# Performance work log

Measured on AMD Instinct MI355X. Metric: run time of the kernel, lower is better.

## Reference

```python
import jax, jax.numpy as jnp
import numpy as np

B, S, D = 4, 2048, 512
H, HD = 8, 64  # head_num, head_dim


def setup_inputs() -> dict:
    key = jax.random.key(0)
    ks = jax.random.split(key, 5)
    scale = 1.0 / np.sqrt(D)  # roughly xavier-scale
    return {
        "x": jax.random.normal(ks[0], (B, S, D), dtype=jnp.float32),
        "Wq": jax.random.normal(ks[1], (D, D), dtype=jnp.float32) * scale,
        "bq": jnp.zeros((D,), dtype=jnp.float32),
        "Wk": jax.random.normal(ks[2], (D, D), dtype=jnp.float32) * scale,
        "bk": jnp.zeros((D,), dtype=jnp.float32),
        "Wv": jax.random.normal(ks[3], (D, D), dtype=jnp.float32) * scale,
        "bv": jnp.zeros((D,), dtype=jnp.float32),
        "Wo": jax.random.normal(ks[4], (D, D), dtype=jnp.float32) * scale,
        "bo": jnp.zeros((D,), dtype=jnp.float32),
    }


def reference(x, Wq, bq, Wk, bk, Wv, bv, Wo, bo):
    b, s, _ = x.shape
    # torch Linear: y = x @ W.T + b; reshape to (b, heads, s, head_dim)
    def proj(W, bias):
        return (x @ W.T + bias).reshape(b, s, H, HD).transpose(0, 2, 1, 3)
    Q, K, V = proj(Wq, bq), proj(Wk, bk), proj(Wv, bv)
    inv_sqrt_dk = 1.0 / jnp.sqrt(jnp.float32(HD))
    scores = jnp.einsum("bhqd,bhkd->bhqk", Q, K) * inv_sqrt_dk
    attn = jax.nn.softmax(scores, axis=-1)  # F.softmax default -> last dim
    ctx = jnp.einsum("bhqk,bhkd->bhqd", attn, V)
    ctx = ctx.transpose(0, 2, 1, 3).reshape(b, s, D)
    return ctx @ Wo.T + bo
```

## Files before the change

### kernel.cpp

```cpp
#include <hip/hip_runtime.h>
#include <hip/hip_bf16.h>
#include <cstdint>
#include <cstddef>

#define S_LEN 2048
#define D_DIM 512
#define NHEAD 8
#define HDIM  64

typedef __attribute__((ext_vector_type(8)))  __bf16 b8;
typedef __attribute__((ext_vector_type(4)))  __bf16 b4;
typedef __attribute__((ext_vector_type(4)))  float  f4;
typedef __attribute__((ext_vector_type(16))) float  f16v;
typedef __attribute__((ext_vector_type(4)))  unsigned int u32x4;

#define AS_GLOBAL __attribute__((address_space(1)))
#define AS_LDS    __attribute__((address_space(3)))

__device__ __forceinline__ void load_lds16(const void* g, void* l) {
  __builtin_amdgcn_global_load_lds((const AS_GLOBAL void*)g, (AS_LDS void*)l, 16, 0, 0);
}

__device__ __forceinline__ f4 mfma16(b8 a, b8 b, f4 c) {
  return __builtin_amdgcn_mfma_f32_16x16x32_bf16(a, b, c, 0, 0, 0);
}
__device__ __forceinline__ f16v mfma32(b8 a, b8 b, f16v c) {
  return __builtin_amdgcn_mfma_f32_32x32x16_bf16(a, b, c, 0, 0, 0);
}

__device__ __forceinline__ float exp2v(float x) {
#if __has_builtin(__builtin_amdgcn_exp2f)
  return __builtin_amdgcn_exp2f(x);
#else
  float r; asm("v_exp_f32 %0, %1" : "=v"(r) : "v"(x)); return r;
#endif
}

__device__ __forceinline__ unsigned int pkbf(float lo, float hi_) {
  unsigned int r;
  asm("v_cvt_pk_bf16_f32 %0, %1, %2" : "=v"(r) : "v"(lo), "v"(hi_));
  return r;
}

__device__ __forceinline__ float xhalf_max(float v) {
  return fmaxf(v, __shfl_xor(v, 32));
}
__device__ __forceinline__ float xhalf_add(float v) {
  return v + __shfl_xor(v, 32);
}

__device__ __forceinline__ b8 lds_frag(const __bf16* base, int row, int bc) {
  return *reinterpret_cast<const b8*>((const char*)base + row * 128 + (bc ^ ((row & 7) << 4)));
}

__global__ __launch_bounds__(256) void cvt_kernel(const float* __restrict__ in,
                                                  __bf16* __restrict__ out) {
  int i = (blockIdx.x * 256 + threadIdx.x) * 4;
  float4 v = *reinterpret_cast<const float4*>(in + i);
  b4 o;
  o.x = (__bf16)v.x; o.y = (__bf16)v.y; o.z = (__bf16)v.z; o.w = (__bf16)v.w;
  *reinterpret_cast<b4*>(out + i) = o;
}

__global__ __launch_bounds__(256) void cvt_w_kernel(const float* __restrict__ w0, const float* __restrict__ w1,
                                                    const float* __restrict__ w2, const float* __restrict__ w3,
                                                    __bf16* o0, __bf16* o1, __bf16* o2, __bf16* o3) {
  const float* in = blockIdx.y == 0 ? w0 : blockIdx.y == 1 ? w1 : blockIdx.y == 2 ? w2 : w3;
  __bf16* out     = blockIdx.y == 0 ? o0 : blockIdx.y == 1 ? o1 : blockIdx.y == 2 ? o2 : o3;
  int i = (blockIdx.x * 256 + threadIdx.x) * 4;
  float4 v = *reinterpret_cast<const float4*>(in + i);
  b4 o;
  o.x = (__bf16)v.x; o.y = (__bf16)v.y; o.z = (__bf16)v.z; o.w = (__bf16)v.w;
  *reinterpret_cast<b4*>(out + i) = o;
}

__device__ __forceinline__ void gemm_core(const __bf16* __restrict__ A, const __bf16* __restrict__ W,
                                          int m0, int n0, __bf16* As, __bf16* Bs, f4 acc[4][4]) {
  const int t = threadIdx.x;
  const int lane = t & 63;
  const int w = t >> 6, wr = w >> 1, wc = w & 1;
  const f4 zero = {0.f, 0.f, 0.f, 0.f};
  #pragma unroll
  for (int mi = 0; mi < 4; ++mi)
    #pragma unroll
    for (int ni = 0; ni < 4; ++ni) acc[mi][ni] = zero;

  const char* Ab = (const char*)A;
  const char* Wb = (const char*)W;
  for (int kt = 0; kt < 512; kt += 64) {
    __syncthreads();
    #pragma unroll
    for (int i = 0; i < 4; ++i) {
      int o = i * 4096 + t * 16;
      int row = o >> 7, cb = o & 127;
      int scb = cb ^ ((row & 7) << 4);
      load_lds16(Ab + ((size_t)(m0 + row) * 512 + kt) * 2 + scb, (char*)As + o);
      load_lds16(Wb + ((size_t)(n0 + row) * 512 + kt) * 2 + scb, (char*)Bs + o);
    }
    __syncthreads();
    #pragma unroll
    for (int kk = 0; kk < 2; ++kk) {
      b8 af[4], bf[4];
      #pragma unroll
      for (int mi = 0; mi < 4; ++mi)
        af[mi] = lds_frag(As, wr * 64 + mi * 16 + (lane & 15), kk * 64 + ((lane >> 4) << 4));
      #pragma unroll
      for (int ni = 0; ni < 4; ++ni)
        bf[ni] = lds_frag(Bs, wc * 64 + ni * 16 + (lane & 15), kk * 64 + ((lane >> 4) << 4));
      #pragma unroll
      for (int mi = 0; mi < 4; ++mi)
        #pragma unroll
        for (int ni = 0; ni < 4; ++ni)
          acc[mi][ni] = mfma16(af[mi], bf[ni], acc[mi][ni]);
    }
  }
}

__global__ __launch_bounds__(256) void gemm_qkv_kernel(
    const __bf16* __restrict__ xb,
    const __bf16* __restrict__ wq, const __bf16* __restrict__ wk, const __bf16* __restrict__ wv,
    const float* __restrict__ bq, const float* __restrict__ bk, const float* __restrict__ bv,
    __bf16* Qo, __bf16* Ko, __bf16* Vo) {
  __shared__ __bf16 As[128 * 64];
  __shared__ __bf16 Bs[128 * 64];
  int z = blockIdx.z;
  const __bf16* W = z == 0 ? wq : (z == 1 ? wk : wv);
  const float* bias = z == 0 ? bq : (z == 1 ? bk : bv);
  __bf16* out = z == 0 ? Qo : (z == 1 ? Ko : Vo);
  const float sc = (z == 0) ? 0.18033688011112042f : 1.0f;
  int m0 = blockIdx.x * 128, n0 = blockIdx.y * 128;
  f4 acc[4][4];
  gemm_core(xb, W, m0, n0, As, Bs, acc);
  int t = threadIdx.x, lane = t & 63, w = t >> 6, wr = w >> 1, wc = w & 1;
  #pragma unroll
  for (int mi = 0; mi < 4; ++mi)
    #pragma unroll
    for (int ni = 0; ni < 4; ++ni)
      #pragma unroll
      for (int r = 0; r < 4; ++r) {
        int m = m0 + wr * 64 + mi * 16 + ((lane >> 4) << 2) + r;
        int n = n0 + wc * 64 + ni * 16 + (lane & 15);
        float v = (acc[mi][ni][r] + bias[n]) * sc;
        int b = m >> 11, s = m & 2047, h = n >> 6, hd = n & 63;
        out[(((size_t)(b * NHEAD + h)) * S_LEN + s) * HDIM + hd] = (__bf16)v;
      }
}

__global__ __launch_bounds__(256) void gemm_o_kernel(const __bf16* __restrict__ ctx,
                                                     const __bf16* __restrict__ wo,
                                                     const float* __restrict__ bo,
                                                     float* __restrict__ out) {
  __shared__ __bf16 As[128 * 64];
  __shared__ __bf16 Bs[128 * 64];
  int m0 = blockIdx.x * 128, n0 = blockIdx.y * 128;
  f4 acc[4][4];
  gemm_core(ctx, wo, m0, n0, As, Bs, acc);
  int t = threadIdx.x, lane = t & 63, w = t >> 6, wr = w >> 1, wc = w & 1;
  #pragma unroll
  for (int mi = 0; mi < 4; ++mi)
    #pragma unroll
    for (int ni = 0; ni < 4; ++ni)
      #pragma unroll
      for (int r = 0; r < 4; ++r) {
        int m = m0 + wr * 64 + mi * 16 + ((lane >> 4) << 2) + r;
        int n = n0 + wc * 64 + ni * 16 + (lane & 15);
        out[(size_t)m * D_DIM + n] = acc[mi][ni][r] + bo[n];
      }
}

__global__ __launch_bounds__(256) void transpose_v_kernel(const __bf16* __restrict__ V,
                                                          __bf16* __restrict__ Vt) {
  __shared__ __bf16 tile[64][72];
  int bh = blockIdx.y, s0 = blockIdx.x * 64;
  const __bf16* Vp = V + (size_t)bh * S_LEN * HDIM;
  __bf16* Vtp = Vt + (size_t)bh * HDIM * S_LEN;
  int t = threadIdx.x;
  #pragma unroll
  for (int i = 0; i < 4; ++i) {
    int q = t + i * 256;
    int row = q >> 4, c4 = (q & 15) * 4;
    b4 v = *reinterpret_cast<const b4*>(&Vp[(size_t)(s0 + row) * HDIM + c4]);
    *reinterpret_cast<b4*>(&tile[row][c4]) = v;
  }
  __syncthreads();
  #pragma unroll
  for (int i = 0; i < 4; ++i) {
    int q = t + i * 256;
    int d = q >> 4, s4 = (q & 15) * 4;
    b4 v;
    v.x = tile[s4 + 0][d]; v.y = tile[s4 + 1][d];
    v.z = tile[s4 + 2][d]; v.w = tile[s4 + 3][d];
    *reinterpret_cast<b4*>(&Vtp[(size_t)d * S_LEN + s0 + s4]) = v;
  }
}

#define NTG 16

#define MKFRAG(dst, st, base) do {                                   \
    unsigned int A0_ = pkbf((st)[(base)+0], (st)[(base)+1]);         \
    unsigned int A1_ = pkbf((st)[(base)+2], (st)[(base)+3]);         \
    unsigned int B0_ = pkbf((st)[(base)+4], (st)[(base)+5]);         \
    unsigned int B1_ = pkbf((st)[(base)+6], (st)[(base)+7]);         \
    asm("v_permlane32_swap_b32 %0, %1" : "+v"(A0_), "+v"(B0_));      \
    asm("v_permlane32_swap_b32 %0, %1" : "+v"(A1_), "+v"(B1_));      \
    u32x4 wv_; wv_.x = A0_; wv_.y = A1_; wv_.z = B0_; wv_.w = B1_;   \
    dst = __builtin_bit_cast(b8, wv_);                               \
  } while (0)

#define TILE(KO, VO) do {                                                     \
    f16v t0 = Z16, t1 = Z16;                                                  \
    __builtin_amdgcn_s_setprio(1);                                            \
    _Pragma("unroll")                                                         \
    for (int ks = 0; ks < 4; ++ks) {                                          \
      b8 kf0 = *reinterpret_cast<const AS_LDS b8*>(sb + koff[ks] + (KO));     \
      b8 kf1 = *reinterpret_cast<const AS_LDS b8*>(sb + koff[ks] + (KO) + 4096); \
      t0 = mfma32(kf0, qf[ks], t0);                                           \
      t1 = mfma32(kf1, qf[ks], t1);                                           \
    }                                                                         \
    __builtin_amdgcn_s_setprio(0);                                            \
    float a0 = fmaxf(fmaxf(t0[0], t0[8]),  fmaxf(t1[0], t1[8]));              \
    float a1 = fmaxf(fmaxf(t0[1], t0[9]),  fmaxf(t1[1], t1[9]));              \
    float a2 = fmaxf(fmaxf(t0[2], t0[10]), fmaxf(t1[2], t1[10]));             \
    float a3 = fmaxf(fmaxf(t0[3], t0[11]), fmaxf(t1[3], t1[11]));             \
    float a4 = fmaxf(fmaxf(t0[4], t0[12]), fmaxf(t1[4], t1[12]));             \
    float a5 = fmaxf(fmaxf(t0[5], t0[13]), fmaxf(t1[5], t1[13]));             \
    float a6 = fmaxf(fmaxf(t0[6], t0[14]), fmaxf(t1[6], t1[14]));             \
    float a7 = fmaxf(fmaxf(t0[7], t0[15]), fmaxf(t1[7], t1[15]));             \
    float mx = fmaxf(fmaxf(fmaxf(a0, a1), fmaxf(a2, a3)),                     \
                     fmaxf(fmaxf(a4, a5), fmaxf(a6, a7)));                    \
    mx = xhalf_max(mx);                                                       \
    if (!__all(mx - mr <= 11.5f)) {                                           \
      float mn = fmaxf(mr, mx);                                               \
      float al = exp2v(mr - mn);                                              \
      mr = mn; lsum *= al; o0 *= al; o1 *= al;                                \
    }                                                                         \
    _Pragma("unroll")                                                         \
    for (int r = 0; r < 16; ++r) t0[r] = exp2v(t0[r] - mr);                   \
    _Pragma("unroll")                                                         \
    for (int r = 0; r < 16; ++r) t1[r] = exp2v(t1[r] - mr);                   \
    {                                                                         \
      float p0 = (t0[0] + t1[0]) + (t0[8]  + t1[8]);                          \
      float p1 = (t0[1] + t1[1]) + (t0[9]  + t1[9]);                          \
      float p2 = (t0[2] + t1[2]) + (t0[10] + t1[10]);                         \
      float p3 = (t0[3] + t1[3]) + (t0[11] + t1[11]);                         \
      float p4 = (t0[4] + t1[4]) + (t0[12] + t1[12]);                         \
      float p5 = (t0[5] + t1[5]) + (t0[13] + t1[13]);                         \
      float p6 = (t0[6] + t1[6]) + (t0[14] + t1[14]);                         \
      float p7 = (t0[7] + t1[7]) + (t0[15] + t1[15]);                         \
      lsum += ((p0 + p1) + (p2 + p3)) + ((p4 + p5) + (p6 + p7));              \
    }                                                                         \
    __builtin_amdgcn_s_setprio(1);                                            \
    _Pragma("unroll")                                                         \
    for (int ks = 0; ks < 4; ++ks) {                                          \
      b8 pa;                                                                  \
      if (ks == 0)      MKFRAG(pa, t0, 0);                                    \
      else if (ks == 1) MKFRAG(pa, t0, 8);                                    \
      else if (ks == 2) MKFRAG(pa, t1, 0);                                    \
      else              MKFRAG(pa, t1, 8);                                    \
      b8 vf0 = *reinterpret_cast<const AS_LDS b8*>(sb + koff[ks] + (VO));     \
      b8 vf1 = *reinterpret_cast<const AS_LDS b8*>(sb + koff[ks] + (VO) + 4096); \
      o0 = mfma32(vf0, pa, o0);                                               \
      o1 = mfma32(vf1, pa, o1);                                               \
    }                                                                         \
    __builtin_amdgcn_s_setprio(0);                                            \
  } while (0)

__global__ __launch_bounds__(512, 4) void attn_kernel(const __bf16* __restrict__ Q,
                                                      const __bf16* __restrict__ K,
                                                      const __bf16* __restrict__ Vt,
                                                      __bf16* __restrict__ ctx) {
  __shared__ char smem_[65536];
  int t = threadIdx.x, lane = t & 63, w = t >> 6;
  int lane31 = lane & 31, hi = lane >> 5;
  int grp = w >> 2, qs = w & 3, t256 = t & 255;

  int bid = blockIdx.x;
  int nid = (bid & 7) * 64 + (bid >> 3);
  int bh = nid >> 4, qtile = nid & 15;
  int b = bh >> 3, h = bh & 7;
  int q = qtile * 128 + qs * 32 + lane31;
  const __bf16* Qp = Q + (size_t)bh * S_LEN * HDIM;
  const __bf16* Kp = K + (size_t)bh * S_LEN * HDIM;
  const __bf16* Vp = Vt + (size_t)bh * HDIM * S_LEN;
  const int kv0 = grp * (S_LEN / 2);

  b8 qf[4];
  #pragma unroll
  for (int ks = 0; ks < 4; ++ks)
    qf[ks] = *reinterpret_cast<const b8*>(&Qp[(size_t)q * HDIM + ks * 16 + hi * 8]);

  const AS_LDS char* sb = (const AS_LDS char*)smem_;
  unsigned koff[4];
  #pragma unroll
  for (int ks = 0; ks < 4; ++ks) {
    int bc = hi * 16 + ks * 32;
    koff[ks] = grp * 16384 + lane31 * 128 + (bc ^ ((lane31 & 7) << 4));
  }

  int oA = t256 * 16, oB = 4096 + t256 * 16;
  int rA = oA >> 7, rB = oB >> 7;
  int sA = (oA & 127) ^ ((rA & 7) << 4), sB = (oB & 127) ^ ((rB & 7) << 4);
  const char* KgA = (const char*)Kp + (size_t)(kv0 + rA) * 128 + sA;
  const char* KgB = (const char*)Kp + (size_t)(kv0 + rB) * 128 + sB;
  const char* VgA = (const char*)Vp + (size_t)rA * (S_LEN * 2) + (size_t)kv0 * 2 + sA;
  const char* VgB = (const char*)Vp + (size_t)rB * (S_LEN * 2) + (size_t)kv0 * 2 + sB;

  const f16v Z16 = {0,0,0,0,0,0,0,0,0,0,0,0,0,0,0,0};
  f16v o0 = Z16, o1 = Z16;
  float mr = -1e30f, lsum = 0.f;

  auto stage = [&](int buf) {
    char* ldsK = smem_ + grp * 16384 + buf * 8192;
    load_lds16(KgA, ldsK + oA);
    load_lds16(KgB, ldsK + oB);
    load_lds16(VgA, ldsK + 32768 + oA);
    load_lds16(VgB, ldsK + 32768 + oB);
    KgA += 8192; KgB += 8192; VgA += 128; VgB += 128;
  };

  stage(0);
  __syncthreads();

  #pragma unroll 1
  for (int it2 = 0; it2 < NTG / 2; ++it2) {
    stage(1);
    TILE(0, 32768);
    __syncthreads();
    if (it2 < NTG / 2 - 1) stage(0);
    TILE(8192, 40960);
    __syncthreads();
  }

  float l_own = xhalf_add(lsum);
  float* OL = (float*)smem_;
  float* ML = OL + 8192;
  if (grp == 1) {
    #pragma unroll
    for (int g = 0; g < 4; ++g)
      #pragma unroll
      for (int j = 0; j < 4; ++j) {
        int d = 8 * g + 4 * hi + j;
        OL[(qs * 64 + d) * 32 + lane31]      = o0[4 * g + j];
        OL[(qs * 64 + 32 + d) * 32 + lane31] = o1[4 * g + j];
      }
    if (hi == 0) { ML[qs * 32 + lane31] = mr; ML[128 + qs * 32 + lane31] = l_own; }
  }
  __syncthreads();
  if (grp == 0) {
    float m1 = ML[qs * 32 + lane31], l1 = ML[128 + qs * 32 + lane31];
    float mm = fmaxf(mr, m1);
    float s0 = exp2v(mr - mm), s1 = exp2v(m1 - mm);
    float inv = 1.0f / (l_own * s0 + l1 * s1);
    __bf16* cp = ctx + (size_t)b * S_LEN * D_DIM + (size_t)q * D_DIM + (size_t)h * HDIM;
    #pragma unroll
    for (int g = 0; g < 4; ++g) {
      b4 v0, v1;
      #pragma unroll
      for (int j = 0; j < 4; ++j) {
        int d = 8 * g + 4 * hi + j;
        v0[j] = (__bf16)((o0[4 * g + j] * s0 + OL[(qs * 64 + d) * 32 + lane31] * s1) * inv);
        v1[j] = (__bf16)((o1[4 * g + j] * s0 + OL[(qs * 64 + 32 + d) * 32 + lane31] * s1) * inv);
      }
      int d0 = 8 * g + 4 * hi;
      *reinterpret_cast<b4*>(cp + d0)      = v0;
      *reinterpret_cast<b4*>(cp + 32 + d0) = v1;
    }
  }
}

extern "C" void kernel_launch(void* const* d_in, const int* in_sizes, int n_in,
                              void* d_out, int out_size, void* d_ws, size_t ws_size,
                              hipStream_t stream) {
  const float* x  = (const float*)d_in[0];
  const float* Wq = (const float*)d_in[1];
  const float* bq = (const float*)d_in[2];
  const float* Wk = (const float*)d_in[3];
  const float* bk = (const float*)d_in[4];
  const float* Wv = (const float*)d_in[5];
  const float* bv = (const float*)d_in[6];
  const float* Wo = (const float*)d_in[7];
  const float* bo = (const float*)d_in[8];
  float* out = (float*)d_out;

  char* ws = (char*)d_ws;
  __bf16* xb   = (__bf16*)(ws);
  __bf16* wqb  = xb  + 4194304;
  __bf16* wkb  = wqb + 262144;
  __bf16* wvb  = wkb + 262144;
  __bf16* wob  = wvb + 262144;
  __bf16* Qb   = wob + 262144;
  __bf16* Kb   = Qb  + 4194304;
  __bf16* Vb   = Kb  + 4194304;
  __bf16* Vtb  = Vb  + 4194304;
  __bf16* ctxb = xb;

  cvt_kernel<<<dim3(4096), dim3(256), 0, stream>>>(x, xb);
  cvt_w_kernel<<<dim3(256, 4), dim3(256), 0, stream>>>(Wq, Wk, Wv, Wo, wqb, wkb, wvb, wob);
  gemm_qkv_kernel<<<dim3(64, 4, 3), dim3(256), 0, stream>>>(xb, wqb, wkb, wvb, bq, bk, bv, Qb, Kb, Vb);
  transpose_v_kernel<<<dim3(32, 32), dim3(256), 0, stream>>>(Vb, Vtb);
  attn_kernel<<<dim3(512), dim3(512), 0, stream>>>(Qb, Kb, Vtb, ctxb);
  gemm_o_kernel<<<dim3(64, 4), dim3(256), 0, stream>>>(ctxb, wob, bo, out);
}
```

Before: 102.0 us.

## Software-pipeline QK^T of next tile with softmax and PV of current tile

Splits the attention tile into a QK^T stage and a softmax+PV stage and reorders the loop so the scores for the next KV tile are computed before the softmax/PV of the current one. The LDS layout grows to 40 KB per group, with K double-buffered and V triple-buffered, so V data survives one extra iteration. The goal is to overlap MFMA score work with the exp/reduction VALU work and hide LDS latency. In exchange it keeps two extra 16-float score accumulators live, which adds register pressure, and it raises LDS use to 80 KB per block, which may limit occupancy.

```diff
diff --git a/kernel.cpp b/kernel.cpp
--- a/kernel.cpp
+++ b/kernel.cpp
@@ -195,6 +195,7 @@
 }
 
 #define NTG 16
+#define GRPS 40960
 
 #define MKFRAG(dst, st, base) do {                                   \
     unsigned int A0_ = pkbf((st)[(base)+0], (st)[(base)+1]);         \
@@ -207,25 +208,26 @@
     dst = __builtin_bit_cast(b8, wv_);                               \
   } while (0)
 
-#define TILE(KO, VO) do {                                                     \
-    f16v t0 = Z16, t1 = Z16;                                                  \
-    __builtin_amdgcn_s_setprio(1);                                            \
+#define QKT(T0, T1, KO) do {                                                  \
+    T0 = Z16; T1 = Z16;                                                       \
     _Pragma("unroll")                                                         \
     for (int ks = 0; ks < 4; ++ks) {                                          \
       b8 kf0 = *reinterpret_cast<const AS_LDS b8*>(sb + koff[ks] + (KO));     \
       b8 kf1 = *reinterpret_cast<const AS_LDS b8*>(sb + koff[ks] + (KO) + 4096); \
-      t0 = mfma32(kf0, qf[ks], t0);                                           \
-      t1 = mfma32(kf1, qf[ks], t1);                                           \
+      T0 = mfma32(kf0, qf[ks], T0);                                           \
+      T1 = mfma32(kf1, qf[ks], T1);                                           \
     }                                                                         \
-    __builtin_amdgcn_s_setprio(0);                                            \
-    float a0 = fmaxf(fmaxf(t0[0], t0[8]),  fmaxf(t1[0], t1[8]));              \
-    float a1 = fmaxf(fmaxf(t0[1], t0[9]),  fmaxf(t1[1], t1[9]));              \
-    float a2 = fmaxf(fmaxf(t0[2], t0[10]), fmaxf(t1[2], t1[10]));             \
-    float a3 = fmaxf(fmaxf(t0[3], t0[11]), fmaxf(t1[3], t1[11]));             \
-    float a4 = fmaxf(fmaxf(t0[4], t0[12]), fmaxf(t1[4], t1[12]));             \
-    float a5 = fmaxf(fmaxf(t0[5], t0[13]), fmaxf(t1[5], t1[13]));             \
-    float a6 = fmaxf(fmaxf(t0[6], t0[14]), fmaxf(t1[6], t1[14]));             \
-    float a7 = fmaxf(fmaxf(t0[7], t0[15]), fmaxf(t1[7], t1[15]));             \
+  } while (0)
+
+#define SOFTPV(T0, T1, VO) do {                                               \
+    float a0 = fmaxf(fmaxf(T0[0], T0[8]),  fmaxf(T1[0], T1[8]));              \
+    float a1 = fmaxf(fmaxf(T0[1], T0[9]),  fmaxf(T1[1], T1[9]));              \
+    float a2 = fmaxf(fmaxf(T0[2], T0[10]), fmaxf(T1[2], T1[10]));             \
+    float a3 = fmaxf(fmaxf(T0[3], T0[11]), fmaxf(T1[3], T1[11]));             \
+    float a4 = fmaxf(fmaxf(T0[4], T0[12]), fmaxf(T1[4], T1[12]));             \
+    float a5 = fmaxf(fmaxf(T0[5], T0[13]), fmaxf(T1[5], T1[13]));             \
+    float a6 = fmaxf(fmaxf(T0[6], T0[14]), fmaxf(T1[6], T1[14]));             \
+    float a7 = fmaxf(fmaxf(T0[7], T0[15]), fmaxf(T1[7], T1[15]));             \
     float mx = fmaxf(fmaxf(fmaxf(a0, a1), fmaxf(a2, a3)),                     \
                      fmaxf(fmaxf(a4, a5), fmaxf(a6, a7)));                    \
     mx = xhalf_max(mx);                                                       \
@@ -235,28 +237,28 @@
       mr = mn; lsum *= al; o0 *= al; o1 *= al;                                \
     }                                                                         \
     _Pragma("unroll")                                                         \
-    for (int r = 0; r < 16; ++r) t0[r] = exp2v(t0[r] - mr);                   \
+    for (int r = 0; r < 16; ++r) T0[r] = exp2v(T0[r] - mr);                   \
     _Pragma("unroll")                                                         \
-    for (int r = 0; r < 16; ++r) t1[r] = exp2v(t1[r] - mr);                   \
+    for (int r = 0; r < 16; ++r) T1[r] = exp2v(T1[r] - mr);                   \
     {                                                                         \
-      float p0 = (t0[0] + t1[0]) + (t0[8]  + t1[8]);                          \
-      float p1 = (t0[1] + t1[1]) + (t0[9]  + t1[9]);                          \
-      float p2 = (t0[2] + t1[2]) + (t0[10] + t1[10]);                         \
-      float p3 = (t0[3] + t1[3]) + (t0[11] + t1[11]);                         \
-      float p4 = (t0[4] + t1[4]) + (t0[12] + t1[12]);                         \
-      float p5 = (t0[5] + t1[5]) + (t0[13] + t1[13]);                         \
-      float p6 = (t0[6] + t1[6]) + (t0[14] + t1[14]);                         \
-      float p7 = (t0[7] + t1[7]) + (t0[15] + t1[15]);                         \
+      float p0 = (T0[0] + T1[0]) + (T0[8]  + T1[8]);                          \
+      float p1 = (T0[1] + T1[1]) + (T0[9]  + T1[9]);                          \
+      float p2 = (T0[2] + T1[2]) + (T0[10] + T1[10]);                         \
+      float p3 = (T0[3] + T1[3]) + (T0[11] + T1[11]);                         \
+      float p4 = (T0[4] + T1[4]) + (T0[12] + T1[12]);                         \
+      float p5 = (T0[5] + T1[5]) + (T0[13] + T1[13]);                         \
+      float p6 = (T0[6] + T1[6]) + (T0[14] + T1[14]);                         \
+      float p7 = (T0[7] + T1[7]) + (T0[15] + T1[15]);                         \
       lsum += ((p0 + p1) + (p2 + p3)) + ((p4 + p5) + (p6 + p7));              \
     }                                                                         \
     __builtin_amdgcn_s_setprio(1);                                            \
     _Pragma("unroll")                                                         \
     for (int ks = 0; ks < 4; ++ks) {                                          \
       b8 pa;                                                                  \
-      if (ks == 0)      MKFRAG(pa, t0, 0);                                    \
-      else if (ks == 1) MKFRAG(pa, t0, 8);                                    \
-      else if (ks == 2) MKFRAG(pa, t1, 0);                                    \
-      else              MKFRAG(pa, t1, 8);                                    \
+      if (ks == 0)      MKFRAG(pa, T0, 0);                                    \
+      else if (ks == 1) MKFRAG(pa, T0, 8);                                    \
+      else if (ks == 2) MKFRAG(pa, T1, 0);                                    \
+      else              MKFRAG(pa, T1, 8);                                    \
       b8 vf0 = *reinterpret_cast<const AS_LDS b8*>(sb + koff[ks] + (VO));     \
       b8 vf1 = *reinterpret_cast<const AS_LDS b8*>(sb + koff[ks] + (VO) + 4096); \
       o0 = mfma32(vf0, pa, o0);                                               \
@@ -269,7 +271,7 @@
                                                       const __bf16* __restrict__ K,
                                                       const __bf16* __restrict__ Vt,
                                                       __bf16* __restrict__ ctx) {
-  __shared__ char smem_[65536];
+  __shared__ char smem_[2 * GRPS];
   int t = threadIdx.x, lane = t & 63, w = t >> 6;
   int lane31 = lane & 31, hi = lane >> 5;
   int grp = w >> 2, qs = w & 3, t256 = t & 255;
@@ -294,41 +296,55 @@
   #pragma unroll
   for (int ks = 0; ks < 4; ++ks) {
     int bc = hi * 16 + ks * 32;
-    koff[ks] = grp * 16384 + lane31 * 128 + (bc ^ ((lane31 & 7) << 4));
-  }
-
-  int oA = t256 * 16, oB = 4096 + t256 * 16;
-  int rA = oA >> 7, rB = oB >> 7;
-  int sA = (oA & 127) ^ ((rA & 7) << 4), sB = (oB & 127) ^ ((rB & 7) << 4);
+    koff[ks] = grp * GRPS + lane31 * 128 + (bc ^ ((lane31 & 7) << 4));
+  }
+
+  int oA = t256 * 16;
+  int rA = oA >> 7;
+  int sA = (oA & 127) ^ ((rA & 7) << 4);
   const char* KgA = (const char*)Kp + (size_t)(kv0 + rA) * 128 + sA;
-  const char* KgB = (const char*)Kp + (size_t)(kv0 + rB) * 128 + sB;
   const char* VgA = (const char*)Vp + (size_t)rA * (S_LEN * 2) + (size_t)kv0 * 2 + sA;
-  const char* VgB = (const char*)Vp + (size_t)rB * (S_LEN * 2) + (size_t)kv0 * 2 + sB;
 
   const f16v Z16 = {0,0,0,0,0,0,0,0,0,0,0,0,0,0,0,0};
   f16v o0 = Z16, o1 = Z16;
+  f16v c0, c1, n0, n1;
   float mr = -1e30f, lsum = 0.f;
 
-  auto stage = [&](int buf) {
-    char* ldsK = smem_ + grp * 16384 + buf * 8192;
-    load_lds16(KgA, ldsK + oA);
-    load_lds16(KgB, ldsK + oB);
-    load_lds16(VgA, ldsK + 32768 + oA);
-    load_lds16(VgB, ldsK + 32768 + oB);
-    KgA += 8192; KgB += 8192; VgA += 128; VgB += 128;
+  auto stage = [&](unsigned kdo, unsigned vdo) {
+    char* ldsB = smem_ + grp * GRPS;
+    load_lds16(KgA,          ldsB + kdo + oA);
+    load_lds16(KgA + 4096,   ldsB + kdo + oA + 4096);
+    load_lds16(VgA,          ldsB + vdo + oA);
+    load_lds16(VgA + 131072, ldsB + vdo + oA + 4096);
+    KgA += 8192; VgA += 128;
   };
 
-  stage(0);
+  stage(0, 16384);
   __syncthreads();
+  stage(8192, 24576);
+  QKT(c0, c1, 0);
+  __syncthreads();
+
+  unsigned vc = 16384;
+  unsigned vs = 32768;
 
   #pragma unroll 1
-  for (int it2 = 0; it2 < NTG / 2; ++it2) {
-    stage(1);
-    TILE(0, 32768);
+  for (int it2 = 0; it2 < 8; ++it2) {
+    QKT(n0, n1, 8192);
+    if (it2 < 7) stage(0, vs);
+    SOFTPV(c0, c1, vc);
     __syncthreads();
-    if (it2 < NTG / 2 - 1) stage(0);
-    TILE(8192, 40960);
+    vc = (vc == 32768u) ? 16384u : vc + 8192u;
+    vs = (vs == 32768u) ? 16384u : vs + 8192u;
+
+    if (it2 < 7) {
+      QKT(c0, c1, 0);
+      stage(8192, vs);
+    }
+    SOFTPV(n0, n1, vc);
     __syncthreads();
+    vc = (vc == 32768u) ? 16384u : vc + 8192u;
+    vs = (vs == 32768u) ? 16384u : vs + 8192u;
   }
 
   float l_own = xhalf_add(lsum);
```

After: 259.5 us. 154% more time.
